# Optimization experiments

Hardware: AMD Instinct MI355X
Metric: run time of the kernel (lower is better)

The kernel has to match this reference:

```python
import jax, jax.numpy as jnp
import numpy as np
import math
from jax import lax

TSCALE = 256
NUM_SAMPLE = 32
PERBIN = 3
WINDOWS = [4, 8, 16, 32, 64, 128, 192, 256]
RATIO = 0.25
B = 2
DIM = 512
H1 = 256   # hid_dim_1d
H3 = 512   # hid_dim_3d
H2 = 128   # hid_dim_2d


def _bin_mask(xmin, xmax, tscale, num_sample, perbin):
    # exact replica of BEM._get_interp1d_bin_mask (setup-time numpy)
    plen = float(xmax - xmin)
    step = plen / (num_sample * perbin - 1.0)
    samples = [xmin + step * i for i in range(num_sample * perbin)]
    cols = []
    for idx in range(num_sample):
        v = np.zeros([tscale])
        for s in samples[idx * perbin:(idx + 1) * perbin]:
            up = math.ceil(s)
            dec, down = math.modf(s)
            if 0 <= int(down) <= tscale - 1:
                v[int(down)] += 1 - dec
            if 0 <= int(up) <= tscale - 1:
                v[int(up)] += dec
        cols.append(v / perbin)
    return np.stack(cols, axis=1)  # (tscale, num_sample)


def build_sample_mask():
    mats = []
    for w in WINDOWS:
        ws = w + w * RATIO
        vecs = []
        for t in range(TSCALE):
            d = ws * 0.5
            vecs.append(_bin_mask(t - d, t + d, TSCALE, NUM_SAMPLE, PERBIN))
        mats.append(np.stack(vecs, axis=2))  # (T, N, T)
    m = np.stack(mats, axis=3).astype(np.float32)  # (T, N, T, W)
    return jnp.asarray(m.reshape(TSCALE, -1))  # (T, N*T*W)


def gn(x, g, b, groups=32, eps=1e-5):
    Bsz, C = x.shape[0], x.shape[1]
    xr = x.reshape(Bsz, groups, -1)
    mu = xr.mean(-1, keepdims=True)
    var = xr.var(-1, keepdims=True)
    xr = (xr - mu) * lax.rsqrt(var + eps)
    x = xr.reshape(x.shape)
    bshape = (1, C) + (1,) * (x.ndim - 2)
    return x * g.reshape(bshape) + b.reshape(bshape)


def conv(x, w, b, strides, padding, dn):
    y = lax.conv_general_dilated(x, w, strides, padding, dimension_numbers=dn)
    return y + b.reshape((1, -1) + (1,) * (y.ndim - 2))


def setup_inputs() -> dict:
    key = jax.random.key(0)
    ks = jax.random.split(key, 16)

    def w(k, shape, fan):
        return (jax.random.normal(k, shape) * (1.0 / np.sqrt(fan))).astype(jnp.float32)

    inp = {}
    inp['x'] = jax.random.normal(ks[0], (B, DIM, TSCALE), jnp.float32)
    inp['sample_mask'] = build_sample_mask()
    inp['c1_w'] = w(ks[1], (H1, DIM, 3), DIM * 3)
    inp['c1_b'] = jnp.zeros((H1,), jnp.float32)
    inp['gn1_g'] = jnp.ones((H1,), jnp.float32)
    inp['gn1_b'] = jnp.zeros((H1,), jnp.float32)
    inp['r3d_w'] = w(ks[2], (H3, H1, NUM_SAMPLE, 1, 1), H1 * NUM_SAMPLE)
    inp['r3d_b'] = jnp.zeros((H3,), jnp.float32)
    inp['gn3_g'] = jnp.ones((H3,), jnp.float32)
    inp['gn3_b'] = jnp.zeros((H3,), jnp.float32)
    inp['r2d_w'] = w(ks[3], (H2, H3, 1, 1), H3)
    inp['r2d_b'] = jnp.zeros((H2,), jnp.float32)
    inp['gn2_g'] = jnp.ones((H2,), jnp.float32)
    inp['gn2_b'] = jnp.zeros((H2,), jnp.float32)
    inp['s1_w'] = w(ks[4], (H2, H2, 3, 3), H2 * 9)
    inp['s1_b'] = jnp.zeros((H2,), jnp.float32)
    inp['sgn_g'] = jnp.ones((H2,), jnp.float32)
    inp['sgn_b'] = jnp.zeros((H2,), jnp.float32)
    inp['s2_w'] = w(ks[5], (1, H2, 1, 1), H2)
    inp['s2_b'] = jnp.zeros((1,), jnp.float32)
    inp['e1_w'] = w(ks[6], (H2, H2, 3, 3), H2 * 9)
    inp['e1_b'] = jnp.zeros((H2,), jnp.float32)
    inp['egn_g'] = jnp.ones((H2,), jnp.float32)
    inp['egn_b'] = jnp.zeros((H2,), jnp.float32)
    inp['e2_w'] = w(ks[7], (1, H2, 1, 1), H2)
    inp['e2_b'] = jnp.zeros((1,), jnp.float32)
    return inp


def reference(x, sample_mask, c1_w, c1_b, gn1_g, gn1_b, r3d_w, r3d_b, gn3_g, gn3_b,
              r2d_w, r2d_b, gn2_g, gn2_b, s1_w, s1_b, sgn_g, sgn_b, s2_w, s2_b,
              e1_w, e1_b, egn_g, egn_b, e2_w, e2_b):
    relu = jax.nn.relu
    W = len(WINDOWS)
    # conv_1: Unit1D(k=3, same pad) + GN + ReLU  -> (B, H1, T)
    h = relu(gn(conv(x, c1_w, c1_b, (1,), [(1, 1)], ('NCH', 'OIH', 'NCH')), gn1_g, gn1_b))
    Bsz, C, T = h.shape
    # sample: dense GEMM against sparse interp1d mask -> (B, C, N, T, W)
    samp = jnp.matmul(h, sample_mask).reshape(Bsz, C, NUM_SAMPLE, T, W)
    # reduction_layer 'fc': Conv3d over the N axis (kernel=stride=N) + GN + ReLU
    y = conv(samp, r3d_w, r3d_b, (NUM_SAMPLE, 1, 1), 'VALID', ('NCDHW', 'OIDHW', 'NCDHW'))
    y = relu(gn(y, gn3_g, gn3_b))[:, :, 0]  # squeeze depth -> (B, H3, T, W)
    f = relu(gn(conv(y, r2d_w, r2d_b, (1, 1), 'VALID', ('NCHW', 'OIHW', 'NCHW')), gn2_g, gn2_b))

    def head(w1, b1, gg, gb, w2, b2):
        t = relu(gn(conv(f, w1, b1, (1, 1), [(1, 1), (1, 1)], ('NCHW', 'OIHW', 'NCHW')), gg, gb))
        return jax.nn.sigmoid(conv(t, w2, b2, (1, 1), 'VALID', ('NCHW', 'OIHW', 'NCHW')))

    cs = head(s1_w, s1_b, sgn_g, sgn_b, s2_w, s2_b)  # (B,1,T,W)
    ce = head(e1_w, e1_b, egn_g, egn_b, e2_w, e2_b)  # (B,1,T,W)
    return jnp.concatenate([cs, ce], axis=1)  # (B,2,T,W): [start, end]
```

## Files before the change

### kernel.cpp

```cpp
#include <hip/hip_runtime.h>
#include <hip/hip_bf16.h>

typedef __hip_bfloat16 bf16;
typedef __attribute__((ext_vector_type(8))) short short8;
typedef __attribute__((ext_vector_type(4))) float f32x4;

static __device__ __forceinline__ float b2f(bf16 v) { return __bfloat162float(v); }

static __device__ __forceinline__ float ldin(const void* p, long i, int bf) {
    return bf ? b2f(((const bf16*)p)[i]) : ((const float*)p)[i];
}

__global__ void detect_k(const unsigned short* __restrict__ x16, int* __restrict__ flag) {
    __shared__ int cnt[256];
    unsigned short u = x16[threadIdx.x];
    int e = (u >> 7) & 0xFF;
    cnt[threadIdx.x] = (e >= 100 && e <= 140) ? 1 : 0;
    __syncthreads();
    for (int off = 128; off > 0; off >>= 1) {
        if (threadIdx.x < off) cnt[threadIdx.x] += cnt[threadIdx.x + off];
        __syncthreads();
    }
    if (threadIdx.x == 0) *flag = (cnt[0] > 217) ? 1 : 0;
}

__global__ void cast_bf_k(const void* __restrict__ in, bf16* __restrict__ out,
                          int n, const int* __restrict__ flagp) {
    int bf = *flagp;
    int idx = blockIdx.x * 256 + threadIdx.x;
    if (idx >= n) return;
    out[idx] = __float2bfloat16(ldin(in, idx, bf));
}

__global__ __launch_bounds__(256) void transpose_w3b_k(const void* __restrict__ w3,
                                                       bf16* __restrict__ out,
                                                       const int* __restrict__ flagp) {
    int bf = *flagp;
    int h3 = blockIdx.x;
    __shared__ bf16 t[8192];
    long base = (long)h3 * 8192;
    for (int i = threadIdx.x; i < 8192; i += 256)
        t[i] = __float2bfloat16(ldin(w3, base + i, bf));
    __syncthreads();
    for (int i = threadIdx.x; i < 8192; i += 256) {
        int n = i >> 8, c = i & 255;
        out[((long)n * 512 + h3) * 256 + c] = t[c * 32 + n];
    }
}

__global__ void cast_hT_k(const float* __restrict__ h, bf16* __restrict__ out) {
    int idx = blockIdx.x * 256 + threadIdx.x;
    if (idx >= 131072) return;
    int b = idx >> 16, r = idx & 65535;
    int tau = r >> 8, c = r & 255;
    out[idx] = __float2bfloat16(h[b * 65536 + c * 256 + tau]);
}

__global__ __launch_bounds__(256) void castT_k(const float* __restrict__ y,
                                               bf16* __restrict__ yT) {
    int p0 = blockIdx.x * 64, c0 = blockIdx.y * 64, b = blockIdx.z;
    __shared__ bf16 t[64][65];
    const float* src = y + (long)b * 1048576;
    for (int i = threadIdx.x; i < 4096; i += 256) {
        int cl = i >> 6, pl = i & 63;
        t[pl][cl] = __float2bfloat16(src[(long)(c0 + cl) * 2048 + p0 + pl]);
    }
    __syncthreads();
    bf16* dst = yT + (long)b * 1048576;
    for (int i = threadIdx.x; i < 4096; i += 256) {
        int pl = i >> 6, cl = i & 63;
        dst[(long)(p0 + pl) * 512 + c0 + cl] = t[pl][cl];
    }
}

__global__ void im2col_xb_k(const void* __restrict__ x, bf16* __restrict__ out,
                            const int* __restrict__ flagp) {
    int bf = *flagp;
    int idx = blockIdx.x * 256 + threadIdx.x;
    if (idx >= 786432) return;
    int b = idx / 393216;
    int rem = idx - b * 393216;
    int t = rem / 1536, k = rem - t * 1536;
    int c = k / 3, q = k - c * 3;
    int tt = t + q - 1;
    float v = (tt >= 0 && tt < 256) ? ldin(x, ((long)b * 512 + c) * 256 + tt, bf) : 0.f;
    out[idx] = __float2bfloat16(v);
}

__global__ void im2col_fb_k(const float* __restrict__ f, bf16* __restrict__ out) {
    int idx = blockIdx.x * 256 + threadIdx.x;
    if (idx >= 4718592) return;
    int b = idx / 2359296;
    int rem = idx - b * 2359296;
    int p = rem / 1152, k = rem - p * 1152;
    int c = k / 9, q = k - c * 9;
    int dy = q / 3, dx = q - dy * 3;
    int t = p >> 3, w = p & 7;
    int tt = t + dy - 1, ww = w + dx - 1;
    float v = (tt >= 0 && tt < 256 && ww >= 0 && ww < 8)
                  ? f[((long)b * 128 + c) * 2048 + tt * 8 + ww] : 0.f;
    out[idx] = __float2bfloat16(v);
}

template<int NT>
__global__ __launch_bounds__(256) void wgemm_mfma(
    const bf16* __restrict__ A, const bf16* __restrict__ B, float* __restrict__ C,
    const void* __restrict__ bias1, const void* __restrict__ bias2,
    int M, int K, int P, int a_div, long a_zs, const int* __restrict__ flagp)
{
    int bf = *flagp;
    int z = blockIdx.z;
    const bf16* A2 = A + (long)(z / a_div) * a_zs;
    const bf16* B2 = B + (long)(z & 1) * (long)P * K;
    float* C2 = C + (long)z * M * P;
    const void* bi = (z / a_div) ? bias2 : bias1;

    int tid = threadIdx.x;
    int wv = tid >> 6, lane = tid & 63;
    int q = lane >> 4, col = lane & 15;
    int m0 = blockIdx.y * 64 + wv * 16;
    int p0 = blockIdx.x * (16 * NT);

    f32x4 acc[NT];
    #pragma unroll
    for (int i = 0; i < NT; ++i) acc[i] = (f32x4){0.f, 0.f, 0.f, 0.f};

    const short8* Ab = (const short8*)(A2 + (long)(m0 + col) * K);
    int kch = K >> 5;
    for (int kc = 0; kc < kch; ++kc) {
        short8 af = Ab[kc * 4 + q];
        #pragma unroll
        for (int nt = 0; nt < NT; ++nt) {
            const short8* Bb = (const short8*)(B2 + (long)(p0 + nt * 16 + col) * K);
            short8 bfr = Bb[kc * 4 + q];
            acc[nt] = __builtin_amdgcn_mfma_f32_16x16x32_bf16(af, bfr, acc[nt], 0, 0, 0);
        }
    }

    float bv[4];
    #pragma unroll
    for (int r = 0; r < 4; ++r) bv[r] = ldin(bi, m0 + q * 4 + r, bf);
    #pragma unroll
    for (int nt = 0; nt < NT; ++nt)
        #pragma unroll
        for (int r = 0; r < 4; ++r)
            C2[(long)(m0 + q * 4 + r) * P + p0 + nt * 16 + col] = acc[nt][r] + bv[r];
}

__global__ __launch_bounds__(256) void pgemm_mfma(
    const bf16* __restrict__ w3b, const bf16* __restrict__ hbT,
    float* __restrict__ P)
{
    int z = blockIdx.z;
    int b = z >> 5, n = z & 31;
    int bm = blockIdx.y;
    int tid = threadIdx.x;
    int wv = tid >> 6, lane = tid & 63;
    int q = lane >> 4, col = lane & 15;

    f32x4 acc[16];
    #pragma unroll
    for (int i = 0; i < 16; ++i) acc[i] = (f32x4){0.f, 0.f, 0.f, 0.f};

    const short8* Abase = (const short8*)(w3b + ((long)n * 512 + bm * 64 + wv * 16 + col) * 256);
    const short8* Bbase = (const short8*)(hbT + (long)b * 65536);

    #pragma unroll
    for (int kc = 0; kc < 8; ++kc) {
        short8 af = Abase[kc * 4 + q];
        #pragma unroll
        for (int nt = 0; nt < 16; ++nt) {
            short8 bfr = Bbase[(nt * 16 + col) * 32 + kc * 4 + q];
            acc[nt] = __builtin_amdgcn_mfma_f32_16x16x32_bf16(af, bfr, acc[nt], 0, 0, 0);
        }
    }

    long dbase = (long)b * 4194304 + (long)n * 256 +
                 (long)(bm * 64 + wv * 16 + q * 4) * 8192 + col;
    #pragma unroll
    for (int nt = 0; nt < 16; ++nt)
        #pragma unroll
        for (int r = 0; r < 4; ++r)
            P[dbase + (long)r * 8192 + nt * 16] = acc[nt][r];
}

__global__ __launch_bounds__(1024) void gn_relu_k(
    float* __restrict__ buf, const void* __restrict__ g, const void* __restrict__ bt,
    int C, int S, int groups, const int* __restrict__ flagp)
{
    int bf = *flagp;
    int nt = blockDim.x;
    int gid = blockIdx.x;
    int b = gid / groups, gr = gid % groups;
    int cpg = C / groups;
    long cnt = (long)cpg * S;
    float* base = buf + ((long)b * C + (long)gr * cpg) * S;
    double s = 0.0, s2 = 0.0;
    for (long i = threadIdx.x; i < cnt; i += nt) {
        float v = base[i];
        s += v; s2 += (double)v * v;
    }
    __shared__ double rs[1024], rq[1024];
    rs[threadIdx.x] = s; rq[threadIdx.x] = s2;
    __syncthreads();
    for (int off = nt >> 1; off > 0; off >>= 1) {
        if (threadIdx.x < off) { rs[threadIdx.x] += rs[threadIdx.x + off]; rq[threadIdx.x] += rq[threadIdx.x + off]; }
        __syncthreads();
    }
    double mean_d = rs[0] / (double)cnt;
    float mean = (float)mean_d;
    float var = (float)(rq[0] / (double)cnt - mean_d * mean_d);
    float rstd = rsqrtf(var + 1e-5f);
    for (long i = threadIdx.x; i < cnt; i += nt) {
        int c = gr * cpg + (int)(i / S);
        float v = (base[i] - mean) * rstd * ldin(g, c, bf) + ldin(bt, c, bf);
        base[i] = v > 0.f ? v : 0.f;
    }
}

__global__ __launch_bounds__(256) void gn_part_k(
    const float* __restrict__ buf, double* __restrict__ part,
    int C, int S, int groups, int chunks)
{
    int gi = blockIdx.x / chunks, ch = blockIdx.x % chunks;
    int b = gi / groups, gr = gi % groups;
    int cpg = C / groups;
    long cnt = (long)cpg * S;
    long clen = cnt / chunks;
    const float* base = buf + ((long)b * C + (long)gr * cpg) * S + (long)ch * clen;
    double s = 0.0, s2 = 0.0;
    for (long i = threadIdx.x; i < clen; i += 256) {
        float v = base[i];
        s += v; s2 += (double)v * v;
    }
    __shared__ double rs[256], rq[256];
    rs[threadIdx.x] = s; rq[threadIdx.x] = s2;
    __syncthreads();
    for (int off = 128; off > 0; off >>= 1) {
        if (threadIdx.x < off) { rs[threadIdx.x] += rs[threadIdx.x + off]; rq[threadIdx.x] += rq[threadIdx.x + off]; }
        __syncthreads();
    }
    if (threadIdx.x == 0) { part[blockIdx.x * 2] = rs[0]; part[blockIdx.x * 2 + 1] = rq[0]; }
}

__global__ __launch_bounds__(256) void gn_apply_k(
    float* __restrict__ buf, const double* __restrict__ part,
    const void* __restrict__ g, const void* __restrict__ bt,
    int C, int S, int groups, int chunks, const int* __restrict__ flagp)
{
    int bf = *flagp;
    int gi = blockIdx.x / chunks, ch = blockIdx.x % chunks;
    int b = gi / groups, gr = gi % groups;
    int cpg = C / groups;
    long cnt = (long)cpg * S;
    long clen = cnt / chunks;
    double s = 0.0, s2 = 0.0;
    for (int k = 0; k < chunks; ++k) {
        s += part[(gi * chunks + k) * 2];
        s2 += part[(gi * chunks + k) * 2 + 1];
    }
    double mean_d = s / (double)cnt;
    float mean = (float)mean_d;
    float var = (float)(s2 / (double)cnt - mean_d * mean_d);
    float rstd = rsqrtf(var + 1e-5f);
    float* base = buf + ((long)b * C + (long)gr * cpg) * S + (long)ch * clen;
    long off0 = (long)ch * clen;
    for (long i = threadIdx.x; i < clen; i += 256) {
        int c = gr * cpg + (int)((off0 + i) / S);
        float v = (base[i] - mean) * rstd * ldin(g, c, bf) + ldin(bt, c, bf);
        base[i] = v > 0.f ? v : 0.f;
    }
}

__global__ __launch_bounds__(384) void build_table_k(
    const void* __restrict__ mask, int* __restrict__ tabd,
    float* __restrict__ tabw, const int* __restrict__ flagp)
{
    int bf = *flagp;
    int nw = blockIdx.x;
    int w = nw >> 5, n = nw & 31;
    int tid = threadIdx.x;
    int d = tid - 165;
    float v = 0.f;
    if (d <= 165) {
        if (d < 0) v = ldin(mask, (long)(254 + d) * 65536 + ((long)n * 256 + 254) * 8 + w, bf);
        else       v = ldin(mask, (long)(1 + d) * 65536 + ((long)n * 256 + 1) * 8 + w, bf);
    }
    __shared__ unsigned char nz[384];
    nz[tid] = (v != 0.f) ? 1 : 0;
    if (tid < 6) { tabd[nw * 6 + tid] = 0; tabw[nw * 6 + tid] = 0.f; }
    __syncthreads();
    if (v != 0.f) {
        int slot = 0;
        for (int j = 0; j < tid; ++j) slot += nz[j];
        if (slot < 6) { tabd[nw * 6 + slot] = d; tabw[nw * 6 + slot] = v; }
    }
}

__global__ void build_corr_k(const void* __restrict__ mask, const int* __restrict__ tabd,
                             const float* __restrict__ tabw, float* __restrict__ corrB,
                             const int* __restrict__ flagp) {
    int bf = *flagp;
    int idx = blockIdx.x * 256 + threadIdx.x;
    if (idx >= 65536) return;
    int n = idx >> 11, p = idx & 2047;
    int t = p >> 3, w = p & 7;
    float mv = ldin(mask, ((long)n * 256 + t) * 8 + w, bf);
    float sub = 0.f;
    int base = (w * 32 + n) * 6;
    for (int k = 0; k < 6; ++k)
        if (tabd[base + k] == -t && tabw[base + k] != 0.f) sub += tabw[base + k];
    corrB[idx] = mv - sub;
}

__global__ __launch_bounds__(256) void apply_y_k(
    const float* __restrict__ P, const int* __restrict__ tabd,
    const float* __restrict__ tabw, float* __restrict__ part,
    const int* __restrict__ flagp)
{
    int bx = blockIdx.x;
    int h3 = bx >> 1, half = bx & 1;
    int n0 = half * 16;
    __shared__ float2 Pl2[16 * 256];
    __shared__ float4 Tp4[384];
    const float4* p04 = (const float4*)(P + ((long)h3 * 32 + n0) * 256);
    const float4* p14 = (const float4*)(P + ((long)(512 + h3) * 32 + n0) * 256);
    float4* pl4 = (float4*)Pl2;
    for (int i = threadIdx.x; i < 1024; i += 256) {
        float4 a = p04[i], b = p14[i];
        pl4[i * 2]     = make_float4(a.x, b.x, a.y, b.y);
        pl4[i * 2 + 1] = make_float4(a.z, b.z, a.w, b.w);
    }
    float2* tp2 = (float2*)Tp4;
    for (int i = threadIdx.x; i < 768; i += 256) {
        int el = i / 6, k = i - el * 6;
        int ge = ((el >> 4) << 5) + n0 + (el & 15);
        tp2[i] = make_float2(tabw[ge * 6 + k], __int_as_float(tabd[ge * 6 + k]));
    }
    __syncthreads();

    int t = threadIdx.x;
    float a0[8], a1[8];
    #pragma unroll
    for (int w = 0; w < 8; ++w) { a0[w] = 0.f; a1[w] = 0.f; }

    #pragma unroll 1
    for (int nl = 0; nl < 16; ++nl) {
        const float2* Pn = Pl2 + (nl << 8);
        #pragma unroll
        for (int w = 0; w < 8; ++w) {
            int e4 = ((w << 4) + nl) * 3;
            float4 q0 = Tp4[e4], q1 = Tp4[e4 + 1], q2 = Tp4[e4 + 2];
            float wts[6] = {q0.x, q0.z, q1.x, q1.z, q2.x, q2.z};
            int   dss[6] = {__float_as_int(q0.y), __float_as_int(q0.w),
                            __float_as_int(q1.y), __float_as_int(q1.w),
                            __float_as_int(q2.y), __float_as_int(q2.w)};
            #pragma unroll
            for (int k = 0; k < 6; ++k) {
                int tau = t + dss[k];
                int idx = tau & 255;
                float wt = ((unsigned)tau < 256u) ? wts[k] : 0.f;
                float2 pv = Pn[idx];
                a0[w] += wt * pv.x;
                a1[w] += wt * pv.y;
            }
        }
    }

    long y0 = (long)half * 2097152 + (long)h3 * 2048 + (long)t * 8;
    long y1 = y0 + 512L * 2048;
    *(float4*)(part + y0)     = make_float4(a0[0], a0[1], a0[2], a0[3]);
    *(float4*)(part + y0 + 4) = make_float4(a0[4], a0[5], a0[6], a0[7]);
    *(float4*)(part + y1)     = make_float4(a1[0], a1[1], a1[2], a1[3]);
    *(float4*)(part + y1 + 4) = make_float4(a1[4], a1[5], a1[6], a1[7]);
}

__global__ void merge_y_k(const float* __restrict__ part, const float* __restrict__ P,
                          const float* __restrict__ corrB, float* __restrict__ y,
                          const void* __restrict__ r3b, const int* __restrict__ flagp) {
    int bf = *flagp;
    int i = blockIdx.x * 256 + threadIdx.x;
    if (i >= 524288) return;
    const float4* p4 = (const float4*)part;
    float4 a = p4[i], b = p4[i + 524288];
    long e = (long)i * 4;
    int bb_ = (int)(e >> 20);
    int h3 = (int)((e >> 11) & 511);
    int p = (int)(e & 2047);
    float bias = ldin(r3b, h3, bf);
    float4 acc = make_float4(a.x + b.x + bias, a.y + b.y + bias,
                             a.z + b.z + bias, a.w + b.w + bias);
    const float* p0 = P + ((long)(bb_ * 512 + h3) * 32) * 256;
    #pragma unroll 4
    for (int n = 0; n < 32; ++n) {
        float pv = p0[n * 256];
        float4 cb = *(const float4*)(corrB + n * 2048 + p);
        acc.x += pv * cb.x; acc.y += pv * cb.y;
        acc.z += pv * cb.z; acc.w += pv * cb.w;
    }
    ((float4*)y)[i] = acc;
}

__global__ __launch_bounds__(64) void head_out_k(
    const float* __restrict__ t1s, const float* __restrict__ t1e,
    const void* __restrict__ s2w, const void* __restrict__ s2b,
    const void* __restrict__ e2w, const void* __restrict__ e2b,
    void* __restrict__ out, const int* __restrict__ flagp) {
    int bf = *flagp;
    int idx = blockIdx.x * 64 + threadIdx.x;
    if (idx >= 4096) return;
    int b = idx >> 11, p = idx & 2047;
    const float* ts = t1s + (long)b * 262144 + p;
    const float* te = t1e + (long)b * 262144 + p;
    float as = ldin(s2b, 0, bf), ae = ldin(e2b, 0, bf);
    #pragma unroll 8
    for (int c = 0; c < 128; ++c) {
        as += ldin(s2w, c, bf) * ts[(long)c * 2048];
        ae += ldin(e2w, c, bf) * te[(long)c * 2048];
    }
    float vs = 1.f / (1.f + expf(-as));
    float ve = 1.f / (1.f + expf(-ae));
    long o0 = ((long)b * 2) * 2048 + p;
    long o1 = ((long)b * 2 + 1) * 2048 + p;
    if (bf) {
        ((bf16*)out)[o0] = __float2bfloat16(vs);
        ((bf16*)out)[o1] = __float2bfloat16(ve);
    } else {
        ((float*)out)[o0] = vs;
        ((float*)out)[o1] = ve;
    }
}

extern "C" void kernel_launch(void* const* d_in, const int* in_sizes, int n_in,
                              void* d_out, int out_size, void* d_ws, size_t ws_size,
                              hipStream_t stream) {
    const void* x    = d_in[0];
    const void* mask = d_in[1];
    const void* c1w  = d_in[2];
    const void* c1b  = d_in[3];
    const void* gn1g = d_in[4];
    const void* gn1b = d_in[5];
    const void* w3   = d_in[6];
    const void* r3b  = d_in[7];
    const void* gn3g = d_in[8];
    const void* gn3b = d_in[9];
    const void* w2   = d_in[10];
    const void* r2b  = d_in[11];
    const void* gn2g = d_in[12];
    const void* gn2b = d_in[13];
    const void* s1w  = d_in[14];
    const void* s1b  = d_in[15];
    const void* sgng = d_in[16];
    const void* sgnb = d_in[17];
    const void* s2w  = d_in[18];
    const void* s2b  = d_in[19];
    const void* e1w  = d_in[20];
    const void* e1b  = d_in[21];
    const void* egng = d_in[22];
    const void* egnb = d_in[23];
    const void* e2w  = d_in[24];
    const void* e2b  = d_in[25];
    float* ws = (float*)d_ws;

    int*   flagI = (int*)(ws + 0);
    float* h     = ws + 64;
    float* c1t   = ws + 131136;
    float* w2t   = ws + 524352;
    float* s1t   = ws + 589888;
    float* corrB = ws + 884800;
    float* tabw  = ws + 950336;
    int*   tabd  = (int*)(ws + 951872);
    float* t1s   = ws + 986176;
    float* t1e   = ws + 1510464;
    float* f     = ws + 2034752;
    float* y     = ws + 2559040;
    float* w3reg = ws + 4656192;
    float* Pb    = ws + 8850496;
    double* gnbuf = (double*)(ws + 17239104);
    bf16*  w3b   = (bf16*)w3reg;
    bf16*  hbT   = (bf16*)(w3reg + 2097152);
    bf16*  c1wb  = (bf16*)c1t;
    bf16*  w2b   = (bf16*)w2t;
    bf16*  hwb   = (bf16*)s1t;
    bf16*  colxb = (bf16*)y;
    bf16*  fcolb = (bf16*)Pb;
    bf16*  yT    = (bf16*)(Pb + 4194304);
    float* ypart = w3reg;

    dim3 blk(256);
    dim3 blkG(1024);

    detect_k<<<dim3(1), blk, 0, stream>>>((const unsigned short*)x, flagI);

    cast_bf_k<<<dim3(1536), blk, 0, stream>>>(c1w, c1wb, 393216, flagI);
    cast_bf_k<<<dim3(576),  blk, 0, stream>>>(s1w, hwb, 147456, flagI);
    cast_bf_k<<<dim3(576),  blk, 0, stream>>>(e1w, hwb + 147456, 147456, flagI);
    cast_bf_k<<<dim3(256),  blk, 0, stream>>>(w2, w2b, 65536, flagI);
    transpose_w3b_k<<<dim3(512), blk, 0, stream>>>(w3, w3b, flagI);
    build_table_k<<<dim3(256), dim3(384), 0, stream>>>(mask, tabd, tabw, flagI);
    build_corr_k<<<dim3(256), blk, 0, stream>>>(mask, tabd, tabw, corrB, flagI);

    im2col_xb_k<<<dim3(3072), blk, 0, stream>>>(x, colxb, flagI);
    wgemm_mfma<1><<<dim3(16, 4, 2), blk, 0, stream>>>(
        c1wb, colxb, h, c1b, c1b, 256, 1536, 256, 1, 0L, flagI);
    gn_relu_k<<<dim3(64), blkG, 0, stream>>>(h, gn1g, gn1b, 256, 256, 32, flagI);

    cast_hT_k<<<dim3(512), blk, 0, stream>>>(h, hbT);
    pgemm_mfma<<<dim3(1, 8, 64), blk, 0, stream>>>(w3b, hbT, Pb);

    apply_y_k<<<dim3(1024), blk, 0, stream>>>(Pb, tabd, tabw, ypart, flagI);
    merge_y_k<<<dim3(2048), blk, 0, stream>>>(ypart, Pb, corrB, y, r3b, flagI);
    gn_part_k<<<dim3(512), blk, 0, stream>>>(y, gnbuf, 512, 2048, 32, 8);
    gn_apply_k<<<dim3(512), blk, 0, stream>>>(y, gnbuf, gn3g, gn3b, 512, 2048, 32, 8, flagI);

    castT_k<<<dim3(32, 8, 2), blk, 0, stream>>>(y, yT);
    wgemm_mfma<2><<<dim3(64, 2, 2), blk, 0, stream>>>(
        w2b, yT, f, r2b, r2b, 128, 512, 2048, 2, 0L, flagI);
    gn_part_k<<<dim3(256), blk, 0, stream>>>(f, gnbuf, 128, 2048, 32, 4);
    gn_apply_k<<<dim3(256), blk, 0, stream>>>(f, gnbuf, gn2g, gn2b, 128, 2048, 32, 4, flagI);

    im2col_fb_k<<<dim3(18432), blk, 0, stream>>>(f, fcolb);
    wgemm_mfma<4><<<dim3(32, 2, 4), blk, 0, stream>>>(
        hwb, fcolb, t1s, s1b, e1b, 128, 1152, 2048, 2, 147456L, flagI);
    gn_part_k<<<dim3(256), blk, 0, stream>>>(t1s, gnbuf, 128, 2048, 32, 4);
    gn_apply_k<<<dim3(256), blk, 0, stream>>>(t1s, gnbuf, sgng, sgnb, 128, 2048, 32, 4, flagI);
    gn_part_k<<<dim3(256), blk, 0, stream>>>(t1e, gnbuf, 128, 2048, 32, 4);
    gn_apply_k<<<dim3(256), blk, 0, stream>>>(t1e, gnbuf, egng, egnb, 128, 2048, 32, 4, flagI);

    head_out_k<<<dim3(64), dim3(64), 0, stream>>>(t1s, t1e, s2w, s2b, e2w, e2b, d_out, flagI);
}
```

Measured before the change: 433.7 us.

## Fuse sparse-tap apply and correction merge into a single apply_y2 kernel

Merges apply_y_k and merge_y_k into one kernel where each 1024-thread block handles two h3 channels for both batches across all 32 samples and all 8 windows. The partial-sum buffer write and re-read and one launch go away. Zero-weight taps are now skipped with early-exit branches, and the correction term is applied from a transposed corrT layout. Output is staged through shared memory for coalesced stores. In exchange the grid shrinks to 256 blocks and adds chunked LDS loads with extra synchronization, which may lower parallelism.

New measurement: 409.7 us. 1.06x faster.

```diff
diff --git a/kernel.cpp b/kernel.cpp
--- a/kernel.cpp
+++ b/kernel.cpp
@@ -298,107 +298,133 @@
 }
 
 __global__ void build_corr_k(const void* __restrict__ mask, const int* __restrict__ tabd,
-                             const float* __restrict__ tabw, float* __restrict__ corrB,
+                             const float* __restrict__ tabw, float* __restrict__ corrT,
                              const int* __restrict__ flagp) {
     int bf = *flagp;
     int idx = blockIdx.x * 256 + threadIdx.x;
     if (idx >= 65536) return;
-    int n = idx >> 11, p = idx & 2047;
-    int t = p >> 3, w = p & 7;
+    int e = idx >> 8, t = idx & 255;
+    int w = e >> 5, n = e & 31;
     float mv = ldin(mask, ((long)n * 256 + t) * 8 + w, bf);
     float sub = 0.f;
-    int base = (w * 32 + n) * 6;
+    int base = e * 6;
     for (int k = 0; k < 6; ++k)
         if (tabd[base + k] == -t && tabw[base + k] != 0.f) sub += tabw[base + k];
-    corrB[idx] = mv - sub;
-}
-
-__global__ __launch_bounds__(256) void apply_y_k(
+    corrT[idx] = mv - sub;
+}
+
+__global__ __launch_bounds__(1024) void apply_y2_k(
     const float* __restrict__ P, const int* __restrict__ tabd,
-    const float* __restrict__ tabw, float* __restrict__ part,
+    const float* __restrict__ tabw, const float* __restrict__ corrT,
+    float* __restrict__ y, const void* __restrict__ r3b,
     const int* __restrict__ flagp)
 {
-    int bx = blockIdx.x;
-    int h3 = bx >> 1, half = bx & 1;
-    int n0 = half * 16;
-    __shared__ float2 Pl2[16 * 256];
-    __shared__ float4 Tp4[384];
-    const float4* p04 = (const float4*)(P + ((long)h3 * 32 + n0) * 256);
-    const float4* p14 = (const float4*)(P + ((long)(512 + h3) * 32 + n0) * 256);
-    float4* pl4 = (float4*)Pl2;
-    for (int i = threadIdx.x; i < 1024; i += 256) {
-        float4 a = p04[i], b = p14[i];
-        pl4[i * 2]     = make_float4(a.x, b.x, a.y, b.y);
-        pl4[i * 2 + 1] = make_float4(a.z, b.z, a.w, b.w);
-    }
-    float2* tp2 = (float2*)Tp4;
-    for (int i = threadIdx.x; i < 768; i += 256) {
-        int el = i / 6, k = i - el * 6;
-        int ge = ((el >> 4) << 5) + n0 + (el & 15);
-        tp2[i] = make_float2(tabw[ge * 6 + k], __int_as_float(tabd[ge * 6 + k]));
-    }
-    __syncthreads();
-
-    int t = threadIdx.x;
-    float a0[8], a1[8];
-    #pragma unroll
-    for (int w = 0; w < 8; ++w) { a0[w] = 0.f; a1[w] = 0.f; }
-
+    int hp = blockIdx.x;
+    int h0 = hp * 2;
+    int tid = threadIdx.x;
+    int t = tid & 255;
+    int wg = tid >> 8;
+    int w0 = wg * 2;
+
+    __shared__ float4 Pl[12 * 256];
+    __shared__ float4 Tab[768];
+    __shared__ float4 pzv[32];
+
+    const float* Pb00 = P + (long)h0 * 8192;
+    const float* Pb01 = P + (long)(h0 + 1) * 8192;
+    const float* Pb10 = Pb00 + 4194304;
+    const float* Pb11 = Pb01 + 4194304;
+
+    float2* tab2 = (float2*)Tab;
+    for (int i = tid; i < 1536; i += 1024)
+        tab2[i] = make_float2(tabw[i], __int_as_float(tabd[i]));
+    if (tid < 32) {
+        int n = tid;
+        pzv[n] = make_float4(Pb00[n * 256], Pb01[n * 256], Pb10[n * 256], Pb11[n * 256]);
+    }
+
+    float4 acc0 = make_float4(0.f, 0.f, 0.f, 0.f);
+    float4 acc1 = make_float4(0.f, 0.f, 0.f, 0.f);
+
+    int cn0 = 0;
     #pragma unroll 1
-    for (int nl = 0; nl < 16; ++nl) {
-        const float2* Pn = Pl2 + (nl << 8);
-        #pragma unroll
-        for (int w = 0; w < 8; ++w) {
-            int e4 = ((w << 4) + nl) * 3;
-            float4 q0 = Tp4[e4], q1 = Tp4[e4 + 1], q2 = Tp4[e4 + 2];
-            float wts[6] = {q0.x, q0.z, q1.x, q1.z, q2.x, q2.z};
-            int   dss[6] = {__float_as_int(q0.y), __float_as_int(q0.w),
-                            __float_as_int(q1.y), __float_as_int(q1.w),
-                            __float_as_int(q2.y), __float_as_int(q2.w)};
-            #pragma unroll
-            for (int k = 0; k < 6; ++k) {
-                int tau = t + dss[k];
-                int idx = tau & 255;
-                float wt = ((unsigned)tau < 256u) ? wts[k] : 0.f;
-                float2 pv = Pn[idx];
-                a0[w] += wt * pv.x;
-                a1[w] += wt * pv.y;
+    for (int ch = 0; ch < 3; ++ch) {
+        int NC = (ch == 2) ? 8 : 12;
+        __syncthreads();
+        for (int pos = tid; pos < NC * 256; pos += 1024) {
+            int nl = pos >> 8, tau = pos & 255;
+            long o = (long)(cn0 + nl) * 256 + tau;
+            Pl[pos] = make_float4(Pb00[o], Pb01[o], Pb10[o], Pb11[o]);
+        }
+        __syncthreads();
+
+        #pragma unroll 1
+        for (int nl = 0; nl < NC; ++nl) {
+            const float4* Pn = Pl + (nl << 8);
+            auto tap = [&](float wt, float df, float4& acc) {
+                int d = __float_as_int(df);
+                int tau = t + d;
+                float wtk = ((unsigned)tau < 256u) ? wt : 0.f;
+                float4 pv = Pn[tau & 255];
+                acc.x += wtk * pv.x; acc.y += wtk * pv.y;
+                acc.z += wtk * pv.z; acc.w += wtk * pv.w;
+            };
+            int e0 = w0 * 32 + cn0 + nl;
+            {
+                float4 q0 = Tab[e0 * 3], q1 = Tab[e0 * 3 + 1], q2 = Tab[e0 * 3 + 2];
+                if (q0.x != 0.f) { tap(q0.x, q0.y, acc0);
+                 if (q0.z != 0.f) { tap(q0.z, q0.w, acc0);
+                  if (q1.x != 0.f) { tap(q1.x, q1.y, acc0);
+                   if (q1.z != 0.f) { tap(q1.z, q1.w, acc0);
+                    if (q2.x != 0.f) { tap(q2.x, q2.y, acc0);
+                     if (q2.z != 0.f) { tap(q2.z, q2.w, acc0); }}}}}}
+            }
+            {
+                int e1 = e0 + 32;
+                float4 q0 = Tab[e1 * 3], q1 = Tab[e1 * 3 + 1], q2 = Tab[e1 * 3 + 2];
+                if (q0.x != 0.f) { tap(q0.x, q0.y, acc1);
+                 if (q0.z != 0.f) { tap(q0.z, q0.w, acc1);
+                  if (q1.x != 0.f) { tap(q1.x, q1.y, acc1);
+                   if (q1.z != 0.f) { tap(q1.z, q1.w, acc1);
+                    if (q2.x != 0.f) { tap(q2.x, q2.y, acc1);
+                     if (q2.z != 0.f) { tap(q2.z, q2.w, acc1); }}}}}}
             }
         }
-    }
-
-    long y0 = (long)half * 2097152 + (long)h3 * 2048 + (long)t * 8;
-    long y1 = y0 + 512L * 2048;
-    *(float4*)(part + y0)     = make_float4(a0[0], a0[1], a0[2], a0[3]);
-    *(float4*)(part + y0 + 4) = make_float4(a0[4], a0[5], a0[6], a0[7]);
-    *(float4*)(part + y1)     = make_float4(a1[0], a1[1], a1[2], a1[3]);
-    *(float4*)(part + y1 + 4) = make_float4(a1[4], a1[5], a1[6], a1[7]);
-}
-
-__global__ void merge_y_k(const float* __restrict__ part, const float* __restrict__ P,
-                          const float* __restrict__ corrB, float* __restrict__ y,
-                          const void* __restrict__ r3b, const int* __restrict__ flagp) {
-    int bf = *flagp;
-    int i = blockIdx.x * 256 + threadIdx.x;
-    if (i >= 524288) return;
-    const float4* p4 = (const float4*)part;
-    float4 a = p4[i], b = p4[i + 524288];
-    long e = (long)i * 4;
-    int bb_ = (int)(e >> 20);
-    int h3 = (int)((e >> 11) & 511);
-    int p = (int)(e & 2047);
-    float bias = ldin(r3b, h3, bf);
-    float4 acc = make_float4(a.x + b.x + bias, a.y + b.y + bias,
-                             a.z + b.z + bias, a.w + b.w + bias);
-    const float* p0 = P + ((long)(bb_ * 512 + h3) * 32) * 256;
+        cn0 += NC;
+    }
+
+    __syncthreads();
+
+    int bf = *flagp;
+    float g0 = ldin(r3b, h0, bf), g1 = ldin(r3b, h0 + 1, bf);
+    acc0.x += g0; acc0.y += g1; acc0.z += g0; acc0.w += g1;
+    acc1.x += g0; acc1.y += g1; acc1.z += g0; acc1.w += g1;
+
+    const float* cT0 = corrT + (long)w0 * 8192 + t;
+    const float* cT1 = cT0 + 8192;
     #pragma unroll 4
     for (int n = 0; n < 32; ++n) {
-        float pv = p0[n * 256];
-        float4 cb = *(const float4*)(corrB + n * 2048 + p);
-        acc.x += pv * cb.x; acc.y += pv * cb.y;
-        acc.z += pv * cb.z; acc.w += pv * cb.w;
-    }
-    ((float4*)y)[i] = acc;
+        float4 pz = pzv[n];
+        float c0 = cT0[n * 256], c1 = cT1[n * 256];
+        acc0.x += c0 * pz.x; acc0.y += c0 * pz.y;
+        acc0.z += c0 * pz.z; acc0.w += c0 * pz.w;
+        acc1.x += c1 * pz.x; acc1.y += c1 * pz.y;
+        acc1.z += c1 * pz.z; acc1.w += c1 * pz.w;
+    }
+
+    float* yb = (float*)Pl;
+    *(float2*)&yb[0 * 2048 + t * 8 + w0] = make_float2(acc0.x, acc1.x);
+    *(float2*)&yb[1 * 2048 + t * 8 + w0] = make_float2(acc0.y, acc1.y);
+    *(float2*)&yb[2 * 2048 + t * 8 + w0] = make_float2(acc0.z, acc1.z);
+    *(float2*)&yb[3 * 2048 + t * 8 + w0] = make_float2(acc0.w, acc1.w);
+    __syncthreads();
+    for (int f = tid; f < 2048; f += 1024) {
+        int c = f >> 9, r = f & 511;
+        int tt = r >> 1, half = r & 1;
+        float4 v = *(const float4*)&yb[c * 2048 + tt * 8 + half * 4];
+        int b = c >> 1, hh = h0 + (c & 1);
+        *(float4*)&y[((long)b * 512 + hh) * 2048 + tt * 8 + half * 4] = v;
+    }
 }
 
 __global__ __launch_bounds__(64) void head_out_k(
@@ -485,7 +511,6 @@
     bf16*  colxb = (bf16*)y;
     bf16*  fcolb = (bf16*)Pb;
     bf16*  yT    = (bf16*)(Pb + 4194304);
-    float* ypart = w3reg;
 
     dim3 blk(256);
     dim3 blkG(1024);
@@ -508,8 +533,7 @@
     cast_hT_k<<<dim3(512), blk, 0, stream>>>(h, hbT);
     pgemm_mfma<<<dim3(1, 8, 64), blk, 0, stream>>>(w3b, hbT, Pb);
 
-    apply_y_k<<<dim3(1024), blk, 0, stream>>>(Pb, tabd, tabw, ypart, flagI);
-    merge_y_k<<<dim3(2048), blk, 0, stream>>>(ypart, Pb, corrB, y, r3b, flagI);
+    apply_y2_k<<<dim3(256), dim3(1024), 0, stream>>>(Pb, tabd, tabw, corrB, y, r3b, flagI);
     gn_part_k<<<dim3(512), blk, 0, stream>>>(y, gnbuf, 512, 2048, 32, 8);
     gn_apply_k<<<dim3(512), blk, 0, stream>>>(y, gnbuf, gn3g, gn3b, 512, 2048, 32, 8, flagI);
 
```
